# Kernel optimization log

Hardware: AMD Instinct MI355X
Metric: run time of the kernel (lower is better)

Reference implementation:

```python
import jax, jax.numpy as jnp
import numpy as np

NEG_SLOPE = 0.2  # PyG GATConv default LeakyReLU slope


def gat_conv(x, edge_index, W, att_src, att_dst, bias):
    """Faithful PyG GATConv (concat=True, add_self_loops=True).
    x: [N, F_in]; W: [F_in, H*C]; att_src/att_dst: [H, C]; bias: [H*C].
    Returns [N, H*C].
    """
    N = x.shape[0]
    H, C = att_src.shape
    loops = jnp.arange(N, dtype=edge_index.dtype)
    src = jnp.concatenate([edge_index[0], loops])  # message sources
    dst = jnp.concatenate([edge_index[1], loops])  # message targets

    h = (x @ W).reshape(N, H, C)                         # [N,H,C]
    a_src = jnp.sum(h * att_src[None], axis=-1)          # [N,H]
    a_dst = jnp.sum(h * att_dst[None], axis=-1)          # [N,H]

    e = jax.nn.leaky_relu(a_src[src] + a_dst[dst], NEG_SLOPE)   # [E,H]
    # segment softmax over incoming edges of each dst node
    m = jax.ops.segment_max(e, dst, num_segments=N)             # [N,H]
    e = jnp.exp(e - m[dst])
    denom = jax.ops.segment_sum(e, dst, num_segments=N)         # [N,H]
    alpha = e / denom[dst]                                      # [E,H]

    msg = h[src] * alpha[:, :, None]                            # [E,H,C]
    out = jax.ops.segment_sum(msg, dst, num_segments=N)         # [N,H,C]
    return out.reshape(N, H * C) + bias


def setup_inputs() -> dict:
    key = jax.random.key(0)
    ks = jax.random.split(key, 12)
    N, F_in, HID, H, CLS = 50000, 128, 64, 4, 40
    E = 800000
    x = jax.random.normal(ks[0], (N, F_in), dtype=jnp.float32)
    edge_index = jax.random.randint(ks[1], (2, E), 0, N, dtype=jnp.int64)
    s = 0.1
    return {
        "x": x,
        "edge_index": edge_index,
        "W1": jax.random.normal(ks[2], (F_in, H * HID), jnp.float32) * s,
        "att_src1": jax.random.normal(ks[3], (H, HID), jnp.float32) * s,
        "att_dst1": jax.random.normal(ks[4], (H, HID), jnp.float32) * s,
        "b1": jnp.zeros((H * HID,), jnp.float32),
        "W2": jax.random.normal(ks[5], (H * HID, H * CLS), jnp.float32) * s,
        "att_src2": jax.random.normal(ks[6], (H, CLS), jnp.float32) * s,
        "att_dst2": jax.random.normal(ks[7], (H, CLS), jnp.float32) * s,
        "b2": jnp.zeros((H * CLS,), jnp.float32),
    }


def reference(x, edge_index, W1, att_src1, att_dst1, b1, W2, att_src2, att_dst2, b2):
    # feature standardization (torch.std is unbiased, ddof=1)
    mean = jnp.mean(x, axis=0)
    std = jnp.std(x, axis=0, ddof=1)
    x = (x - mean) / std
    x = gat_conv(x, edge_index, W1, att_src1, att_dst1, b1)
    x = jax.nn.relu(x)
    # dropout p=0.4 is identity in eval mode
    x = gat_conv(x, edge_index, W2, att_src2, att_dst2, b2)
    return x
```

## Files before the change

### kernel.cpp

```cpp
#include <hip/hip_runtime.h>
#include <math.h>

#define NEG_SLOPE 0.2f

constexpr int F_IN  = 128;
constexpr int HC1   = 256;
constexpr int HC2   = 160;
constexpr int NHEAD = 4;
constexpr int EB    = 2048;
constexpr int NPB   = 256;
constexpr int BCAP  = 8192;

typedef _Float16 h8v __attribute__((ext_vector_type(8)));
typedef _Float16 h4v __attribute__((ext_vector_type(4)));
typedef _Float16 h2v __attribute__((ext_vector_type(2)));
typedef float f4v __attribute__((ext_vector_type(4)));

#define FMIX_LO(acc, pk, wt) \
    asm("v_fma_mix_f32 %0, %1, %2, %0 op_sel:[0,0,0] op_sel_hi:[1,0,0]" \
        : "+v"(acc) : "v"(pk), "v"(wt))
#define FMIX_HI(acc, pk, wt) \
    asm("v_fma_mix_f32 %0, %1, %2, %0 op_sel:[1,0,0] op_sel_hi:[1,0,0]" \
        : "+v"(acc) : "v"(pk), "v"(wt))

__device__ __forceinline__ int edge_val(const void* p, int m64, long long i) {
    if (m64) return (int)((const long long*)p)[i];
    return ((const int*)p)[i];
}

__global__ void detect_kernel(const unsigned int* __restrict__ ei_words, int* __restrict__ mode,
                              float* __restrict__ stats) {
    stats[threadIdx.x] = 0.f;
    __shared__ unsigned int red[256];
    unsigned int v = 0;
    for (int i = 1 + 2 * (int)threadIdx.x; i < 4096; i += 512) v |= ei_words[i];
    red[threadIdx.x] = v;
    __syncthreads();
    for (int off = 128; off > 0; off >>= 1) {
        if (threadIdx.x < off) red[threadIdx.x] |= red[threadIdx.x + off];
        __syncthreads();
    }
    if (threadIdx.x == 0) *mode = (red[0] == 0u) ? 1 : 0;
}

__global__ __launch_bounds__(256) void fused_pre_kernel(
    const void* __restrict__ ei, const int* __restrict__ mode, int E, int nbuck, int nblk1,
    int* __restrict__ hist, const float* __restrict__ x, float* __restrict__ stats, int N,
    const float* __restrict__ W1, const float* __restrict__ aS1, const float* __restrict__ aD1,
    _Float16* __restrict__ B1x, const float* __restrict__ W2, const float* __restrict__ aS2,
    const float* __restrict__ aD2, _Float16* __restrict__ B2x, int nbStats) {
    int b = blockIdx.x;
    if (b < nblk1) {
        __shared__ int lh[256];
        for (int i = threadIdx.x; i < nbuck; i += 256) lh[i] = 0;
        __syncthreads();
        int m = *mode;
        long long e0 = (long long)b * EB;
#pragma unroll
        for (int k = 0; k < EB / 256; k++) {
            long long e = e0 + (int)threadIdx.x + k * 256;
            if (e < E) {
                int d = edge_val(ei, m, (long long)E + e);
                atomicAdd(&lh[d >> 8], 1);
            }
        }
        __syncthreads();
        for (int i = threadIdx.x; i < nbuck; i += 256) hist[(size_t)i * nblk1 + b] = lh[i];
    } else if (b < nblk1 + nbStats) {
        int t = (int)threadIdx.x;
        int c = t & 31;
        int g = t >> 5;
        int r0 = (b - nblk1) * 256;
        int rend = min(r0 + 256, N);
        f4v s = {0.f, 0.f, 0.f, 0.f}, q = {0.f, 0.f, 0.f, 0.f};
        for (int r = r0 + g; r < rend; r += 8) {
            f4v v = *(const f4v*)&x[(long)r * F_IN + 4 * c];
            s += v;
            q += v * v;
        }
        __shared__ f4v sh4[256];
        sh4[t] = s;
        __syncthreads();
        if (t < 32) {
            f4v a = sh4[t];
            for (int g2 = 1; g2 < 8; g2++) a += sh4[g2 * 32 + t];
            atomicAdd(&stats[4 * t + 0], a[0]);
            atomicAdd(&stats[4 * t + 1], a[1]);
            atomicAdd(&stats[4 * t + 2], a[2]);
            atomicAdd(&stats[4 * t + 3], a[3]);
        }
        __syncthreads();
        sh4[t] = q;
        __syncthreads();
        if (t < 32) {
            f4v a = sh4[t];
            for (int g2 = 1; g2 < 8; g2++) a += sh4[g2 * 32 + t];
            atomicAdd(&stats[128 + 4 * t + 0], a[0]);
            atomicAdd(&stats[128 + 4 * t + 1], a[1]);
            atomicAdd(&stats[128 + 4 * t + 2], a[2]);
            atomicAdd(&stats[128 + 4 * t + 3], a[3]);
        }
    } else {
        constexpr int T1 = (HC1 + 16) * F_IN;
        constexpr int T2 = (HC2 + 16) * HC1;
        int idx = (b - nblk1 - nbStats) * 256 + (int)threadIdx.x;
        if (idx < T1) {
            int n = idx / F_IN, k = idx - n * F_IN;
            float v = 0.f;
            if (n < HC1) {
                v = W1[k * HC1 + n];
            } else {
                int n2 = n - HC1;
                if (n2 < 8) {
                    int hd = n2 & 3;
                    const float* a = (n2 < 4) ? aS1 : aD1;
                    for (int c = 0; c < 64; c++) v += W1[k * HC1 + hd * 64 + c] * a[hd * 64 + c];
                }
            }
            B1x[n * F_IN + k] = (_Float16)v;
        } else if (idx < T1 + T2) {
            int i2 = idx - T1;
            int n = i2 / HC1, k = i2 - n * HC1;
            float v = 0.f;
            if (n < HC2) {
                v = W2[k * HC2 + n];
            } else {
                int n2 = n - HC2;
                if (n2 < 8) {
                    int hd = n2 & 3;
                    const float* a = (n2 < 4) ? aS2 : aD2;
                    for (int c = 0; c < 40; c++) v += W2[k * HC2 + hd * 40 + c] * a[hd * 40 + c];
                }
            }
            B2x[n * HC1 + k] = (_Float16)v;
        }
    }
}

__global__ __launch_bounds__(256) void fused_mid_kernel(
    const float* __restrict__ x, const float* __restrict__ stats, _Float16* __restrict__ xs,
    int total4, float invN, float invN1, const int* __restrict__ hist,
    int* __restrict__ colBaseT, int* __restrict__ bucketTotal, int nbuck, int nblk1,
    int nbStd) {
    int b = blockIdx.x;
    if (b < nbStd) {
        int i = b * 256 + (int)threadIdx.x;
        if (i >= total4) return;
        int c = (i * 4) & (F_IN - 1);
        float4 s4 = *(const float4*)&stats[c];
        float4 q4 = *(const float4*)&stats[128 + c];
        float4 v = ((const float4*)x)[i];
        h4v o;
        o[0] = (_Float16)((v.x - s4.x * invN) / sqrtf((q4.x - s4.x * s4.x * invN) * invN1));
        o[1] = (_Float16)((v.y - s4.y * invN) / sqrtf((q4.y - s4.y * s4.y * invN) * invN1));
        o[2] = (_Float16)((v.z - s4.z * invN) / sqrtf((q4.z - s4.z * s4.z * invN) * invN1));
        o[3] = (_Float16)((v.w - s4.w * invN) / sqrtf((q4.w - s4.w * s4.w * invN) * invN1));
        ((h4v*)xs)[i] = o;
    } else {
        int bb = b - nbStd;
        int t = (int)threadIdx.x;
        __shared__ int sh[512];
        __shared__ int wsum[4];
        for (int i = t; i < nblk1; i += 256) sh[i] = hist[(size_t)bb * nblk1 + i];
        __syncthreads();
        int carry = 0;
        for (int base = 0; base < nblk1; base += 256) {
            int idx = base + t;
            int v = (idx < nblk1) ? sh[idx] : 0;
            int lane = t & 63, w = t >> 6;
            int xv = v;
#pragma unroll
            for (int d = 1; d < 64; d <<= 1) {
                int y = __shfl_up(xv, d);
                if (lane >= d) xv += y;
            }
            if (lane == 63) wsum[w] = xv;
            __syncthreads();
            int wb = 0;
            for (int k = 0; k < w; k++) wb += wsum[k];
            int excl = xv - v + wb + carry;
            if (idx < nblk1) colBaseT[(size_t)idx * nbuck + bb] = excl;
            carry += wsum[0] + wsum[1] + wsum[2] + wsum[3];
            __syncthreads();
        }
        if (t == 0) bucketTotal[bb] = carry;
    }
}

__global__ __launch_bounds__(256) void scatter1_kernel(const void* __restrict__ ei,
                                                       const int* __restrict__ mode, int E,
                                                       int nbuck,
                                                       const int* __restrict__ colBaseT,
                                                       int* __restrict__ bucketEdges) {
    __shared__ int cur[256];
    int b = blockIdx.x;
    for (int i = threadIdx.x; i < nbuck; i += 256)
        cur[i] = colBaseT[(size_t)b * nbuck + i];
    __syncthreads();
    int m = *mode;
    long long e0 = (long long)b * EB;
#pragma unroll
    for (int k = 0; k < EB / 256; k++) {
        long long e = e0 + (int)threadIdx.x + k * 256;
        if (e < E) {
            int s = edge_val(ei, m, e);
            int d = edge_val(ei, m, (long long)E + e);
            int bk = d >> 8;
            int r = atomicAdd(&cur[bk], 1);
            bucketEdges[(size_t)bk * BCAP + r] = s | ((d & (NPB - 1)) << 16);
        }
    }
}

__global__ __launch_bounds__(256) void bucket_count_scan_kernel(
    const int* __restrict__ bucketEdges, const int* __restrict__ bucketTotal,
    int* __restrict__ offsets, int* __restrict__ blocksum, int N) {
    __shared__ int c[NPB];
    int b = blockIdx.x, t = threadIdx.x;
    c[t] = 0;
    __syncthreads();
    int cnt = bucketTotal[b];
    const int* be = bucketEdges + (size_t)b * BCAP;
    for (int i = t; i < cnt; i += 256) atomicAdd(&c[(be[i] >> 16) & (NPB - 1)], 1);
    __syncthreads();
    int node = b * NPB + t;
    int v = (node < N) ? c[t] + 1 : 0;
    int lane = t & 63, w = t >> 6;
    int xv = v;
#pragma unroll
    for (int d = 1; d < 64; d <<= 1) {
        int y = __shfl_up(xv, d);
        if (lane >= d) xv += y;
    }
    __shared__ int wsum[4];
    if (lane == 63) wsum[w] = xv;
    __syncthreads();
    int base = 0;
    for (int k = 0; k < w; k++) base += wsum[k];
    int incl = xv + base;
    if (node < N) offsets[node + 1] = incl;
    if (t == 255) blocksum[b] = incl;
}

__global__ void scan_add_kernel(const int* __restrict__ blocksum, int* __restrict__ offsets, int N,
                                int nb) {
    int t = threadIdx.x;
    int v = (t < nb) ? blocksum[t] : 0;
    int lane = t & 63, w = t >> 6;
    int x = v;
#pragma unroll
    for (int d = 1; d < 64; d <<= 1) {
        int y = __shfl_up(x, d);
        if (lane >= d) x += y;
    }
    __shared__ int wsum[4];
    __shared__ int excl[256];
    if (lane == 63) wsum[w] = x;
    __syncthreads();
    int base = 0;
    for (int k = 0; k < w; k++) base += wsum[k];
    excl[t] = x + base - v;
    __syncthreads();
    int myb = excl[blockIdx.x];
    int i = blockIdx.x * 256 + t;
    if (i < N) offsets[i + 1] += myb;
    if (i == 0) offsets[0] = 0;
}

__device__ __forceinline__ void att1_body(int blk, const _Float16* __restrict__ A,
                                          const _Float16* __restrict__ Batt,
                                          float* __restrict__ as_, float* __restrict__ ad_,
                                          int M) {
    constexpr int KT = F_IN / 32;
    int w = threadIdx.x >> 6;
    int l = threadIdx.x & 63;
    int quad = l >> 4, lan = l & 15;
    int row = blk * 64 + w * 16 + lan;
    int arow = min(row, M - 1);
    const _Float16* Aptr = A + (long)arow * F_IN + quad * 8;
    h8v afr[KT], bfr[KT];
#pragma unroll
    for (int k0 = 0; k0 < KT; k0++) afr[k0] = *(const h8v*)(Aptr + k0 * 32);
#pragma unroll
    for (int k0 = 0; k0 < KT; k0++)
        bfr[k0] = *(const h8v*)(Batt + (long)lan * F_IN + k0 * 32 + quad * 8);
    f4v acc = {0.f, 0.f, 0.f, 0.f};
#pragma unroll
    for (int k0 = 0; k0 < KT; k0++)
        acc = __builtin_amdgcn_mfma_f32_16x16x32_f16(afr[k0], bfr[k0], acc, 0, 0, 0);
    int orow = blk * 64 + w * 16 + quad * 4;
#pragma unroll
    for (int r = 0; r < 4; r++) {
        int gr = orow + r;
        if (gr < M) {
            float av = acc[r];
            if (lan < 4)
                as_[gr * 4 + lan] = av;
            else if (lan < 8)
                ad_[gr * 4 + lan - 4] = av;
        }
    }
}

__global__ __launch_bounds__(256) void fused_csr_att1_kernel(
    const int* __restrict__ bucketEdges, const int* __restrict__ bucketTotal,
    const int* __restrict__ offsets, int* __restrict__ csr, int N, int nbuck,
    const _Float16* __restrict__ xs, const _Float16* __restrict__ B1x,
    float* __restrict__ as_, float* __restrict__ ad_) {
    int b = blockIdx.x;
    if (b < nbuck) {
        __shared__ int cur[NPB];
        int t = threadIdx.x;
        int node = b * NPB + t;
        if (node < N) {
            int off = offsets[node];
            csr[off] = node;
            cur[t] = off + 1;
        }
        __syncthreads();
        int cnt = bucketTotal[b];
        const int* be = bucketEdges + (size_t)b * BCAP;
        for (int i = t; i < cnt; i += 256) {
            int v = be[i];
            int pos = atomicAdd(&cur[(v >> 16) & (NPB - 1)], 1);
            csr[pos] = v & 0xFFFF;
        }
    } else {
        att1_body(b - nbuck, xs, B1x + (size_t)HC1 * F_IN, as_, ad_, N);
    }
}

__global__ __launch_bounds__(256, 4) void aggregate_x4_kernel(
    const _Float16* __restrict__ xs, const float* __restrict__ a_src,
    const float* __restrict__ a_dst, const int* __restrict__ offsets,
    const int* __restrict__ csr_src, _Float16* __restrict__ aggx_lo,
    _Float16* __restrict__ aggx_hi, int Ntot) {
    int w = threadIdx.x >> 6, l = threadIdx.x & 63;
    int node = blockIdx.x * 4 + w;
    if (node >= Ntot) return;

    __shared__ __align__(16) int sidx_sh[4][64];
    __shared__ __align__(16) float ew_sh[4][64][4];

    int start = offsets[node], deg = offsets[node + 1] - start;
    float4 adv = ((const float4*)a_dst)[node];
    const char* hbl = (const char*)xs + 4 * l;

    float ds0 = 0.f, ds1 = 0.f, ds2 = 0.f, ds3 = 0.f;
    float a00 = 0.f, a01 = 0.f, a10 = 0.f, a11 = 0.f;
    float a20 = 0.f, a21 = 0.f, a30 = 0.f, a31 = 0.f;

#define X4_EDGE(p, wv)                                   \
    do {                                                 \
        FMIX_LO(a00, p, wv.x); FMIX_HI(a01, p, wv.x);    \
        FMIX_LO(a10, p, wv.y); FMIX_HI(a11, p, wv.y);    \
        FMIX_LO(a20, p, wv.z); FMIX_HI(a21, p, wv.z);    \
        FMIX_LO(a30, p, wv.w); FMIX_HI(a31, p, wv.w);    \
    } while (0)

    for (int base = 0; base < deg; base += 64) {
        int cnt = min(64, deg - base);
        if (l < cnt) {
            int s = csr_src[start + base + l];
            sidx_sh[w][l] = s * (F_IN * 2);
            float4 av = ((const float4*)a_src)[s];
            float e0 = av.x + adv.x, e1 = av.y + adv.y, e2 = av.z + adv.z, e3 = av.w + adv.w;
            e0 = fmaxf(e0, NEG_SLOPE * e0);
            e1 = fmaxf(e1, NEG_SLOPE * e1);
            e2 = fmaxf(e2, NEG_SLOPE * e2);
            e3 = fmaxf(e3, NEG_SLOPE * e3);
            float w0 = __expf(e0), w1 = __expf(e1), w2 = __expf(e2), w3 = __expf(e3);
            *(float4*)ew_sh[w][l] = make_float4(w0, w1, w2, w3);
            ds0 += w0;
            ds1 += w1;
            ds2 += w2;
            ds3 += w3;
        }
        int j = 0;
        for (; j + 3 < cnt; j += 4) {
            int4 o4 = *(const int4*)&sidx_sh[w][j];
            float4 wa = *(const float4*)ew_sh[w][j + 0];
            float4 wb = *(const float4*)ew_sh[w][j + 1];
            float4 wc = *(const float4*)ew_sh[w][j + 2];
            float4 wd = *(const float4*)ew_sh[w][j + 3];
            int p0 = *(const int*)(hbl + o4.x);
            int p1 = *(const int*)(hbl + o4.y);
            int p2 = *(const int*)(hbl + o4.z);
            int p3 = *(const int*)(hbl + o4.w);
            X4_EDGE(p0, wa);
            X4_EDGE(p1, wb);
            X4_EDGE(p2, wc);
            X4_EDGE(p3, wd);
        }
        for (; j < cnt; j++) {
            int off = sidx_sh[w][j];
            float4 wa = *(const float4*)ew_sh[w][j];
            int p0 = *(const int*)(hbl + off);
            X4_EDGE(p0, wa);
        }
    }
#undef X4_EDGE

#pragma unroll
    for (int off = 1; off < 64; off <<= 1) {
        ds0 += __shfl_xor(ds0, off);
        ds1 += __shfl_xor(ds1, off);
        ds2 += __shfl_xor(ds2, off);
        ds3 += __shfl_xor(ds3, off);
    }

    float i0 = 1.0f / ds0, i1 = 1.0f / ds1, i2 = 1.0f / ds2, i3 = 1.0f / ds3;
    h2v hv;
    hv[0] = (_Float16)(a00 * i0);
    hv[1] = (_Float16)(a01 * i0);
    *(h2v*)(aggx_lo + (size_t)node * F_IN + 2 * l) = hv;
    hv[0] = (_Float16)(a10 * i1);
    hv[1] = (_Float16)(a11 * i1);
    *(h2v*)(aggx_lo + ((size_t)Ntot + node) * F_IN + 2 * l) = hv;
    hv[0] = (_Float16)(a20 * i2);
    hv[1] = (_Float16)(a21 * i2);
    *(h2v*)(aggx_hi + (size_t)node * F_IN + 2 * l) = hv;
    hv[0] = (_Float16)(a30 * i3);
    hv[1] = (_Float16)(a31 * i3);
    *(h2v*)(aggx_hi + ((size_t)Ntot + node) * F_IN + 2 * l) = hv;
}

template <int CT0, int CT1>
__device__ __forceinline__ void gemm1b_lds_body(int blk, const _Float16* __restrict__ Ah,
                                                const _Float16* __restrict__ Btx,
                                                _Float16* Bs, const float* __restrict__ bias,
                                                _Float16* __restrict__ C_, int M) {
    constexpr int NC = CT1 - CT0;
    constexpr int KT = F_IN / 32;
    int t = threadIdx.x;
    int w = t >> 6, l = t & 63;
    int quad = l >> 4, lan = l & 15;
    int row = blk * 64 + w * 16 + lan;
    int arow = min(row, M - 1);
    const _Float16* A0 = Ah + (size_t)arow * F_IN + quad * 8;
    const _Float16* A1 = Ah + ((size_t)M + arow) * F_IN + quad * 8;
    h8v af0[KT], af1[KT];
#pragma unroll
    for (int k0 = 0; k0 < KT; k0++) af0[k0] = *(const h8v*)(A0 + k0 * 32);
#pragma unroll
    for (int k0 = 0; k0 < KT; k0++) af1[k0] = *(const h8v*)(A1 + k0 * 32);
#pragma unroll
    for (int jj = 0; jj < NC * KT * 64 / 256; jj++) {
        int j = jj * 256 + t;
        int cik = j >> 6;
        int k0_ = cik % KT, ci_ = cik / KT;
        int jl = j & 63;
        const _Float16* src =
            Btx + (long)((CT0 + ci_) * 16 + (jl & 15)) * F_IN + k0_ * 32 + (jl >> 4) * 8;
        *(h8v*)(Bs + (size_t)j * 8) = *(const h8v*)src;
    }
    __syncthreads();
    f4v acc[NC] = {};
#pragma unroll
    for (int k0 = 0; k0 < KT; k0++)
#pragma unroll
        for (int ci = 0; ci < NC; ci++) {
            h8v bf = *(const h8v*)(Bs + ((size_t)(ci * KT + k0) * 64 + l) * 8);
            h8v af = (ci < 4) ? af0[k0] : af1[k0];
            acc[ci] = __builtin_amdgcn_mfma_f32_16x16x32_f16(af, bf, acc[ci], 0, 0, 0);
        }
    int orow = blk * 64 + w * 16 + quad * 4;
#pragma unroll
    for (int r = 0; r < 4; r++) {
        int gr = orow + r;
        if (gr < M) {
            _Float16* out = C_ + (long)gr * HC1 + lan;
#pragma unroll
            for (int ci = 0; ci < NC; ci++) {
                int ct = CT0 + ci;
                float v = acc[ci][r] + bias[ct * 16 + lan];
                out[ct * 16] = (_Float16)fmaxf(v, 0.f);
            }
        }
    }
}

__global__ __launch_bounds__(256, 3) void gemm1b_kernel(const _Float16* __restrict__ Alo,
                                                        const _Float16* __restrict__ Ahi,
                                                        const _Float16* __restrict__ Btx,
                                                        const float* __restrict__ bias,
                                                        _Float16* __restrict__ C_, int M) {
    __shared__ __align__(16) _Float16 Bs[8 * 4 * 64 * 8];
    int blk = blockIdx.x >> 1;
    if (blockIdx.x & 1)
        gemm1b_lds_body<8, 16>(blk, Ahi, Btx, Bs, bias, C_, M);
    else
        gemm1b_lds_body<0, 8>(blk, Alo, Btx, Bs, bias, C_, M);
}

template <int CT0, int CT1>
__device__ __forceinline__ void gemm2_lds_body(int blk, const _Float16* __restrict__ A,
                                               const _Float16* __restrict__ Btx,
                                               _Float16* Bs, _Float16* __restrict__ C_,
                                               float* __restrict__ as_, float* __restrict__ ad_,
                                               int M) {
    constexpr int NT = HC2 / 16;
    constexpr int NC = CT1 - CT0;
    constexpr int KT = HC1 / 32;
    int t = threadIdx.x;
    int w = t >> 6, l = t & 63;
    int quad = l >> 4, lan = l & 15;
    int row = blk * 64 + w * 16 + lan;
    int arow = min(row, M - 1);
    const _Float16* Aptr = A + (long)arow * HC1 + quad * 8;
    h8v afr[KT];
#pragma unroll
    for (int k0 = 0; k0 < KT; k0++) afr[k0] = *(const h8v*)(Aptr + k0 * 32);
#pragma unroll
    for (int jj = 0; jj < NC * KT * 64 / 256; jj++) {
        int j = jj * 256 + t;
        int cik = j >> 6;
        int k0_ = cik % KT, ci_ = cik / KT;
        int jl = j & 63;
        const _Float16* src =
            Btx + (long)((CT0 + ci_) * 16 + (jl & 15)) * HC1 + k0_ * 32 + (jl >> 4) * 8;
        *(h8v*)(Bs + (size_t)j * 8) = *(const h8v*)src;
    }
    __syncthreads();
    f4v acc[NC] = {};
#pragma unroll
    for (int k0 = 0; k0 < KT; k0++)
#pragma unroll
        for (int ci = 0; ci < NC; ci++) {
            h8v bf = *(const h8v*)(Bs + ((size_t)(ci * KT + k0) * 64 + l) * 8);
            acc[ci] = __builtin_amdgcn_mfma_f32_16x16x32_f16(afr[k0], bf, acc[ci], 0, 0, 0);
        }
    int orow = blk * 64 + w * 16 + quad * 4;
#pragma unroll
    for (int r = 0; r < 4; r++) {
        int gr = orow + r;
        if (gr < M) {
            _Float16* out = C_ + (long)gr * HC2 + lan;
#pragma unroll
            for (int ci = 0; ci < NC; ci++) {
                int ct = CT0 + ci;
                if (ct < NT) out[ct * 16] = (_Float16)acc[ci][r];
            }
            if (CT1 == NT + 1) {
                float av = acc[NC - 1][r];
                if (lan < 4)
                    as_[gr * 4 + lan] = av;
                else if (lan < 8)
                    ad_[gr * 4 + lan - 4] = av;
            }
        }
    }
}

__global__ __launch_bounds__(256, 3) void gemm2_kernel(const _Float16* __restrict__ A,
                                                       const _Float16* __restrict__ B2x,
                                                       _Float16* __restrict__ C_,
                                                       float* __restrict__ as_,
                                                       float* __restrict__ ad_, int M) {
    __shared__ __align__(16) _Float16 Bs[6 * 8 * 64 * 8];
    int blk = blockIdx.x >> 1;
    if (blockIdx.x & 1)
        gemm2_lds_body<5, 11>(blk, A, B2x, Bs, C_, as_, ad_, M);
    else
        gemm2_lds_body<0, 5>(blk, A, B2x, Bs, C_, as_, ad_, M);
}

template <int HC, bool RELU, typename OutT>
__global__ __launch_bounds__(256, 4) void aggregate_kernel(
    const _Float16* __restrict__ hb, const float* __restrict__ a_src,
    const float* __restrict__ a_dst, const int* __restrict__ offsets,
    const int* __restrict__ csr_src, const float* __restrict__ bias, OutT* __restrict__ out,
    int Ntot) {
    constexpr int ACT = HC / 4;
    constexpr int CHPH = HC / NHEAD;
    constexpr bool FULL = (ACT == 64);
    int w = threadIdx.x >> 6, l = threadIdx.x & 63;
    int node = blockIdx.x * 4 + w;
    if (node >= Ntot) return;

    __shared__ __align__(16) int sidx_sh[4][64];
    __shared__ __align__(16) float ew_sh[4][64][4];

    int start = offsets[node], end = offsets[node + 1];
    int deg = end - start;
    float4 adv = ((const float4*)a_dst)[node];
    const int hd = min((4 * l) / CHPH, 3);
    const char* hbl = (const char*)hb + 8 * l;

    float ds0 = 0.f, ds1 = 0.f, ds2 = 0.f, ds3 = 0.f;
    float a0 = 0.f, a1 = 0.f, a2 = 0.f, a3 = 0.f;

    for (int base = 0; base < deg; base += 64) {
        int cnt = min(64, deg - base);
        if (l < cnt) {
            int s = csr_src[start + base + l];
            sidx_sh[w][l] = s * (HC * 2);
            float4 av = ((const float4*)a_src)[s];
            float e0 = av.x + adv.x, e1 = av.y + adv.y, e2 = av.z + adv.z, e3 = av.w + adv.w;
            e0 = fmaxf(e0, NEG_SLOPE * e0);
            e1 = fmaxf(e1, NEG_SLOPE * e1);
            e2 = fmaxf(e2, NEG_SLOPE * e2);
            e3 = fmaxf(e3, NEG_SLOPE * e3);
            float w0 = __expf(e0), w1 = __expf(e1), w2 = __expf(e2), w3 = __expf(e3);
            *(float4*)ew_sh[w][l] = make_float4(w0, w1, w2, w3);
            ds0 += w0;
            ds1 += w1;
            ds2 += w2;
            ds3 += w3;
        }
        int j = 0;
        for (; j + 7 < cnt; j += 8) {
            int4 oa = *(const int4*)&sidx_sh[w][j];
            int4 ob = *(const int4*)&sidx_sh[w][j + 4];
            float w0 = ew_sh[w][j + 0][hd], w1 = ew_sh[w][j + 1][hd];
            float w2 = ew_sh[w][j + 2][hd], w3 = ew_sh[w][j + 3][hd];
            float w4 = ew_sh[w][j + 4][hd], w5 = ew_sh[w][j + 5][hd];
            float w6 = ew_sh[w][j + 6][hd], w7 = ew_sh[w][j + 7][hd];
            if (FULL || l < ACT) {
                int2 p0 = *(const int2*)(hbl + oa.x);
                int2 p1 = *(const int2*)(hbl + oa.y);
                int2 p2 = *(const int2*)(hbl + oa.z);
                int2 p3 = *(const int2*)(hbl + oa.w);
                int2 p4 = *(const int2*)(hbl + ob.x);
                int2 p5 = *(const int2*)(hbl + ob.y);
                int2 p6 = *(const int2*)(hbl + ob.z);
                int2 p7 = *(const int2*)(hbl + ob.w);
                FMIX_LO(a0, p0.x, w0); FMIX_HI(a1, p0.x, w0);
                FMIX_LO(a2, p0.y, w0); FMIX_HI(a3, p0.y, w0);
                FMIX_LO(a0, p1.x, w1); FMIX_HI(a1, p1.x, w1);
                FMIX_LO(a2, p1.y, w1); FMIX_HI(a3, p1.y, w1);
                FMIX_LO(a0, p2.x, w2); FMIX_HI(a1, p2.x, w2);
                FMIX_LO(a2, p2.y, w2); FMIX_HI(a3, p2.y, w2);
                FMIX_LO(a0, p3.x, w3); FMIX_HI(a1, p3.x, w3);
                FMIX_LO(a2, p3.y, w3); FMIX_HI(a3, p3.y, w3);
                FMIX_LO(a0, p4.x, w4); FMIX_HI(a1, p4.x, w4);
                FMIX_LO(a2, p4.y, w4); FMIX_HI(a3, p4.y, w4);
                FMIX_LO(a0, p5.x, w5); FMIX_HI(a1, p5.x, w5);
                FMIX_LO(a2, p5.y, w5); FMIX_HI(a3, p5.y, w5);
                FMIX_LO(a0, p6.x, w6); FMIX_HI(a1, p6.x, w6);
                FMIX_LO(a2, p6.y, w6); FMIX_HI(a3, p6.y, w6);
                FMIX_LO(a0, p7.x, w7); FMIX_HI(a1, p7.x, w7);
                FMIX_LO(a2, p7.y, w7); FMIX_HI(a3, p7.y, w7);
            }
        }
        for (; j + 3 < cnt; j += 4) {
            int4 o4 = *(const int4*)&sidx_sh[w][j];
            float w0 = ew_sh[w][j + 0][hd], w1 = ew_sh[w][j + 1][hd];
            float w2 = ew_sh[w][j + 2][hd], w3 = ew_sh[w][j + 3][hd];
            if (FULL || l < ACT) {
                int2 p0 = *(const int2*)(hbl + o4.x);
                int2 p1 = *(const int2*)(hbl + o4.y);
                int2 p2 = *(const int2*)(hbl + o4.z);
                int2 p3 = *(const int2*)(hbl + o4.w);
                FMIX_LO(a0, p0.x, w0); FMIX_HI(a1, p0.x, w0);
                FMIX_LO(a2, p0.y, w0); FMIX_HI(a3, p0.y, w0);
                FMIX_LO(a0, p1.x, w1); FMIX_HI(a1, p1.x, w1);
                FMIX_LO(a2, p1.y, w1); FMIX_HI(a3, p1.y, w1);
                FMIX_LO(a0, p2.x, w2); FMIX_HI(a1, p2.x, w2);
                FMIX_LO(a2, p2.y, w2); FMIX_HI(a3, p2.y, w2);
                FMIX_LO(a0, p3.x, w3); FMIX_HI(a1, p3.x, w3);
                FMIX_LO(a2, p3.y, w3); FMIX_HI(a3, p3.y, w3);
            }
        }
        for (; j < cnt; j++) {
            int off = sidx_sh[w][j];
            float w0 = ew_sh[w][j][hd];
            if (FULL || l < ACT) {
                int2 p0 = *(const int2*)(hbl + off);
                FMIX_LO(a0, p0.x, w0); FMIX_HI(a1, p0.x, w0);
                FMIX_LO(a2, p0.y, w0); FMIX_HI(a3, p0.y, w0);
            }
        }
    }

#pragma unroll
    for (int off = 1; off < 64; off <<= 1) {
        ds0 += __shfl_xor(ds0, off);
        ds1 += __shfl_xor(ds1, off);
        ds2 += __shfl_xor(ds2, off);
        ds3 += __shfl_xor(ds3, off);
    }

    if (FULL || l < ACT) {
        float dsel = hd == 0 ? ds0 : hd == 1 ? ds1 : hd == 2 ? ds2 : ds3;
        float inv = 1.0f / dsel;
        float4 bv = ((const float4*)bias)[l];
        float r0 = a0 * inv + bv.x;
        float r1 = a1 * inv + bv.y;
        float r2 = a2 * inv + bv.z;
        float r3 = a3 * inv + bv.w;
        if (RELU) {
            r0 = fmaxf(r0, 0.f);
            r1 = fmaxf(r1, 0.f);
            r2 = fmaxf(r2, 0.f);
            r3 = fmaxf(r3, 0.f);
        }
        OutT* op = out + (long)node * HC + 4 * l;
        if (sizeof(OutT) == 2) {
            h4v hv;
            hv[0] = (_Float16)r0;
            hv[1] = (_Float16)r1;
            hv[2] = (_Float16)r2;
            hv[3] = (_Float16)r3;
            *(h4v*)op = hv;
        } else {
            *(float4*)op = make_float4(r0, r1, r2, r3);
        }
    }
}

extern "C" void kernel_launch(void* const* d_in, const int* in_sizes, int n_in, void* d_out,
                              int out_size, void* d_ws, size_t ws_size, hipStream_t stream) {
    const float* x = (const float*)d_in[0];
    const void* ei = d_in[1];
    const float* W1 = (const float*)d_in[2];
    const float* attS1 = (const float*)d_in[3];
    const float* attD1 = (const float*)d_in[4];
    const float* b1 = (const float*)d_in[5];
    const float* W2 = (const float*)d_in[6];
    const float* attS2 = (const float*)d_in[7];
    const float* attD2 = (const float*)d_in[8];
    const float* b2 = (const float*)d_in[9];
    float* out = (float*)d_out;

    int N = in_sizes[0] / F_IN;
    int E = in_sizes[1] / 2;
    int nb = (N + 255) / 256;
    int nw = (N + 3) / 4;
    int nblk1 = (E + EB - 1) / EB;
    int nbuck = (N + NPB - 1) / NPB;

    _Float16* xs_h = (_Float16*)d_ws;
    _Float16* o1h = xs_h + (size_t)N * F_IN;
    _Float16* hb2 = o1h + (size_t)N * HC1;
    _Float16* aggx_hi = hb2 + (size_t)N * HC2;
    _Float16* B1x = aggx_hi + (size_t)N * HC1;
    _Float16* B2x = B1x + (HC1 + 16) * F_IN;
    float* as1 = (float*)(B2x + (HC2 + 16) * HC1);
    float* ad1 = as1 + (size_t)N * NHEAD;
    float* as2 = ad1 + (size_t)N * NHEAD;
    float* ad2 = as2 + (size_t)N * NHEAD;
    float* stats = ad2 + (size_t)N * NHEAD;
    int* offsets = (int*)(stats + 256);
    int* csr = offsets + (N + 4);
    int* blocksum = csr + (E + N);
    int* mode = blocksum + 256;
    int* bucketEdges = (int*)o1h;
    int* hist = bucketEdges + (size_t)nbuck * BCAP;
    int* colBaseT = hist + (size_t)nbuck * nblk1;
    int* bucketTotal = colBaseT + (size_t)nblk1 * nbuck;
    _Float16* aggx_lo = (_Float16*)d_out;

    constexpr int TCV = (HC1 + 16) * F_IN + (HC2 + 16) * HC1;
    int nbConv = (TCV + 255) / 256;
    int total4 = N * F_IN / 4;
    int nbStd = (total4 + 255) / 256;
    int nbG1 = (N + 63) / 64;

    detect_kernel<<<1, 256, 0, stream>>>((const unsigned int*)ei, mode, stats);
    fused_pre_kernel<<<nblk1 + nb + nbConv, 256, 0, stream>>>(
        ei, mode, E, nbuck, nblk1, hist, x, stats, N, W1, attS1, attD1, B1x, W2, attS2, attD2,
        B2x, nb);
    fused_mid_kernel<<<nbStd + nbuck, 256, 0, stream>>>(x, stats, xs_h, total4,
                                                        1.0f / (float)N, 1.0f / (float)(N - 1),
                                                        hist, colBaseT, bucketTotal, nbuck,
                                                        nblk1, nbStd);
    scatter1_kernel<<<nblk1, 256, 0, stream>>>(ei, mode, E, nbuck, colBaseT, bucketEdges);
    bucket_count_scan_kernel<<<nbuck, 256, 0, stream>>>(bucketEdges, bucketTotal, offsets,
                                                        blocksum, N);
    scan_add_kernel<<<nb, 256, 0, stream>>>(blocksum, offsets, N, nb);
    fused_csr_att1_kernel<<<nbuck + nbG1, 256, 0, stream>>>(bucketEdges, bucketTotal, offsets,
                                                            csr, N, nbuck, xs_h, B1x, as1, ad1);
    aggregate_x4_kernel<<<nw, 256, 0, stream>>>(xs_h, as1, ad1, offsets, csr, aggx_lo, aggx_hi,
                                                N);
    gemm1b_kernel<<<nbG1 * 2, 256, 0, stream>>>(aggx_lo, aggx_hi, B1x, b1, o1h, N);
    gemm2_kernel<<<nbG1 * 2, 256, 0, stream>>>(o1h, B2x, hb2, as2, ad2, N);
    aggregate_kernel<HC2, false, float>
        <<<nw, 256, 0, stream>>>(hb2, as2, ad2, offsets, csr, b2, out, N);
}
```

Before: 292.2 us.

## Fuse layer-1 aggregation with per-node projection GEMM via shared memory

```diff
diff --git a/kernel.cpp b/kernel.cpp
--- a/kernel.cpp
+++ b/kernel.cpp
@@ -330,21 +330,18 @@
     }
 }
 
-__global__ __launch_bounds__(256, 4) void aggregate_x4_kernel(
+__global__ __launch_bounds__(256, 4) void aggregate_x4g_kernel(
     const _Float16* __restrict__ xs, const float* __restrict__ a_src,
     const float* __restrict__ a_dst, const int* __restrict__ offsets,
-    const int* __restrict__ csr_src, _Float16* __restrict__ aggx_lo,
-    _Float16* __restrict__ aggx_hi, int Ntot) {
+    const int* __restrict__ csr_src, const _Float16* __restrict__ B1x,
+    const float* __restrict__ bias, _Float16* __restrict__ o1, int Ntot) {
     int w = threadIdx.x >> 6, l = threadIdx.x & 63;
     int node = blockIdx.x * 4 + w;
-    if (node >= Ntot) return;
+    const bool valid = (node < Ntot);
 
     __shared__ __align__(16) int sidx_sh[4][64];
     __shared__ __align__(16) float ew_sh[4][64][4];
-
-    int start = offsets[node], deg = offsets[node + 1] - start;
-    float4 adv = ((const float4*)a_dst)[node];
-    const char* hbl = (const char*)xs + 4 * l;
+    __shared__ __align__(16) _Float16 agg_sh[4][NHEAD][F_IN];
 
     float ds0 = 0.f, ds1 = 0.f, ds2 = 0.f, ds3 = 0.f;
     float a00 = 0.f, a01 = 0.f, a10 = 0.f, a11 = 0.f;
@@ -358,139 +355,102 @@
         FMIX_LO(a30, p, wv.w); FMIX_HI(a31, p, wv.w);    \
     } while (0)
 
-    for (int base = 0; base < deg; base += 64) {
-        int cnt = min(64, deg - base);
-        if (l < cnt) {
-            int s = csr_src[start + base + l];
-            sidx_sh[w][l] = s * (F_IN * 2);
-            float4 av = ((const float4*)a_src)[s];
-            float e0 = av.x + adv.x, e1 = av.y + adv.y, e2 = av.z + adv.z, e3 = av.w + adv.w;
-            e0 = fmaxf(e0, NEG_SLOPE * e0);
-            e1 = fmaxf(e1, NEG_SLOPE * e1);
-            e2 = fmaxf(e2, NEG_SLOPE * e2);
-            e3 = fmaxf(e3, NEG_SLOPE * e3);
-            float w0 = __expf(e0), w1 = __expf(e1), w2 = __expf(e2), w3 = __expf(e3);
-            *(float4*)ew_sh[w][l] = make_float4(w0, w1, w2, w3);
-            ds0 += w0;
-            ds1 += w1;
-            ds2 += w2;
-            ds3 += w3;
-        }
-        int j = 0;
-        for (; j + 3 < cnt; j += 4) {
-            int4 o4 = *(const int4*)&sidx_sh[w][j];
-            float4 wa = *(const float4*)ew_sh[w][j + 0];
-            float4 wb = *(const float4*)ew_sh[w][j + 1];
-            float4 wc = *(const float4*)ew_sh[w][j + 2];
-            float4 wd = *(const float4*)ew_sh[w][j + 3];
-            int p0 = *(const int*)(hbl + o4.x);
-            int p1 = *(const int*)(hbl + o4.y);
-            int p2 = *(const int*)(hbl + o4.z);
-            int p3 = *(const int*)(hbl + o4.w);
-            X4_EDGE(p0, wa);
-            X4_EDGE(p1, wb);
-            X4_EDGE(p2, wc);
-            X4_EDGE(p3, wd);
-        }
-        for (; j < cnt; j++) {
-            int off = sidx_sh[w][j];
-            float4 wa = *(const float4*)ew_sh[w][j];
-            int p0 = *(const int*)(hbl + off);
-            X4_EDGE(p0, wa);
-        }
+    if (valid) {
+        int start = offsets[node], deg = offsets[node + 1] - start;
+        float4 adv = ((const float4*)a_dst)[node];
+        const char* hbl = (const char*)xs + 4 * l;
+
+        for (int base = 0; base < deg; base += 64) {
+            int cnt = min(64, deg - base);
+            if (l < cnt) {
+                int s = csr_src[start + base + l];
+                sidx_sh[w][l] = s * (F_IN * 2);
+                float4 av = ((const float4*)a_src)[s];
+                float e0 = av.x + adv.x, e1 = av.y + adv.y, e2 = av.z + adv.z,
+                      e3 = av.w + adv.w;
+                e0 = fmaxf(e0, NEG_SLOPE * e0);
+                e1 = fmaxf(e1, NEG_SLOPE * e1);
+                e2 = fmaxf(e2, NEG_SLOPE * e2);
+                e3 = fmaxf(e3, NEG_SLOPE * e3);
+                float w0 = __expf(e0), w1 = __expf(e1), w2 = __expf(e2), w3 = __expf(e3);
+                *(float4*)ew_sh[w][l] = make_float4(w0, w1, w2, w3);
+                ds0 += w0;
+                ds1 += w1;
+                ds2 += w2;
+                ds3 += w3;
+            }
+            int j = 0;
+            for (; j + 3 < cnt; j += 4) {
+                int4 o4 = *(const int4*)&sidx_sh[w][j];
+                float4 wa = *(const float4*)ew_sh[w][j + 0];
+                float4 wb = *(const float4*)ew_sh[w][j + 1];
+                float4 wc = *(const float4*)ew_sh[w][j + 2];
+                float4 wd = *(const float4*)ew_sh[w][j + 3];
+                int p0 = *(const int*)(hbl + o4.x);
+                int p1 = *(const int*)(hbl + o4.y);
+                int p2 = *(const int*)(hbl + o4.z);
+                int p3 = *(const int*)(hbl + o4.w);
+                X4_EDGE(p0, wa);
+                X4_EDGE(p1, wb);
+                X4_EDGE(p2, wc);
+                X4_EDGE(p3, wd);
+            }
+            for (; j < cnt; j++) {
+                int off = sidx_sh[w][j];
+                float4 wa = *(const float4*)ew_sh[w][j];
+                int p0 = *(const int*)(hbl + off);
+                X4_EDGE(p0, wa);
+            }
+        }
+
+#pragma unroll
+        for (int off = 1; off < 64; off <<= 1) {
+            ds0 += __shfl_xor(ds0, off);
+            ds1 += __shfl_xor(ds1, off);
+            ds2 += __shfl_xor(ds2, off);
+            ds3 += __shfl_xor(ds3, off);
+        }
+
+        float i0 = 1.0f / ds0, i1 = 1.0f / ds1, i2 = 1.0f / ds2, i3 = 1.0f / ds3;
+        h2v hv;
+        hv[0] = (_Float16)(a00 * i0);
+        hv[1] = (_Float16)(a01 * i0);
+        *(h2v*)&agg_sh[w][0][2 * l] = hv;
+        hv[0] = (_Float16)(a10 * i1);
+        hv[1] = (_Float16)(a11 * i1);
+        *(h2v*)&agg_sh[w][1][2 * l] = hv;
+        hv[0] = (_Float16)(a20 * i2);
+        hv[1] = (_Float16)(a21 * i2);
+        *(h2v*)&agg_sh[w][2][2 * l] = hv;
+        hv[0] = (_Float16)(a30 * i3);
+        hv[1] = (_Float16)(a31 * i3);
+        *(h2v*)&agg_sh[w][3][2 * l] = hv;
     }
 #undef X4_EDGE
 
-#pragma unroll
-    for (int off = 1; off < 64; off <<= 1) {
-        ds0 += __shfl_xor(ds0, off);
-        ds1 += __shfl_xor(ds1, off);
-        ds2 += __shfl_xor(ds2, off);
-        ds3 += __shfl_xor(ds3, off);
-    }
-
-    float i0 = 1.0f / ds0, i1 = 1.0f / ds1, i2 = 1.0f / ds2, i3 = 1.0f / ds3;
-    h2v hv;
-    hv[0] = (_Float16)(a00 * i0);
-    hv[1] = (_Float16)(a01 * i0);
-    *(h2v*)(aggx_lo + (size_t)node * F_IN + 2 * l) = hv;
-    hv[0] = (_Float16)(a10 * i1);
-    hv[1] = (_Float16)(a11 * i1);
-    *(h2v*)(aggx_lo + ((size_t)Ntot + node) * F_IN + 2 * l) = hv;
-    hv[0] = (_Float16)(a20 * i2);
-    hv[1] = (_Float16)(a21 * i2);
-    *(h2v*)(aggx_hi + (size_t)node * F_IN + 2 * l) = hv;
-    hv[0] = (_Float16)(a30 * i3);
-    hv[1] = (_Float16)(a31 * i3);
-    *(h2v*)(aggx_hi + ((size_t)Ntot + node) * F_IN + 2 * l) = hv;
-}
-
-template <int CT0, int CT1>
-__device__ __forceinline__ void gemm1b_lds_body(int blk, const _Float16* __restrict__ Ah,
-                                                const _Float16* __restrict__ Btx,
-                                                _Float16* Bs, const float* __restrict__ bias,
-                                                _Float16* __restrict__ C_, int M) {
-    constexpr int NC = CT1 - CT0;
-    constexpr int KT = F_IN / 32;
-    int t = threadIdx.x;
-    int w = t >> 6, l = t & 63;
-    int quad = l >> 4, lan = l & 15;
-    int row = blk * 64 + w * 16 + lan;
-    int arow = min(row, M - 1);
-    const _Float16* A0 = Ah + (size_t)arow * F_IN + quad * 8;
-    const _Float16* A1 = Ah + ((size_t)M + arow) * F_IN + quad * 8;
-    h8v af0[KT], af1[KT];
-#pragma unroll
-    for (int k0 = 0; k0 < KT; k0++) af0[k0] = *(const h8v*)(A0 + k0 * 32);
-#pragma unroll
-    for (int k0 = 0; k0 < KT; k0++) af1[k0] = *(const h8v*)(A1 + k0 * 32);
-#pragma unroll
-    for (int jj = 0; jj < NC * KT * 64 / 256; jj++) {
-        int j = jj * 256 + t;
-        int cik = j >> 6;
-        int k0_ = cik % KT, ci_ = cik / KT;
-        int jl = j & 63;
-        const _Float16* src =
-            Btx + (long)((CT0 + ci_) * 16 + (jl & 15)) * F_IN + k0_ * 32 + (jl >> 4) * 8;
-        *(h8v*)(Bs + (size_t)j * 8) = *(const h8v*)src;
-    }
-    __syncthreads();
-    f4v acc[NC] = {};
-#pragma unroll
-    for (int k0 = 0; k0 < KT; k0++)
-#pragma unroll
-        for (int ci = 0; ci < NC; ci++) {
-            h8v bf = *(const h8v*)(Bs + ((size_t)(ci * KT + k0) * 64 + l) * 8);
-            h8v af = (ci < 4) ? af0[k0] : af1[k0];
-            acc[ci] = __builtin_amdgcn_mfma_f32_16x16x32_f16(af, bf, acc[ci], 0, 0, 0);
-        }
-    int orow = blk * 64 + w * 16 + quad * 4;
-#pragma unroll
-    for (int r = 0; r < 4; r++) {
-        int gr = orow + r;
-        if (gr < M) {
-            _Float16* out = C_ + (long)gr * HC1 + lan;
-#pragma unroll
-            for (int ci = 0; ci < NC; ci++) {
-                int ct = CT0 + ci;
-                float v = acc[ci][r] + bias[ct * 16 + lan];
-                out[ct * 16] = (_Float16)fmaxf(v, 0.f);
-            }
-        }
-    }
-}
-
-__global__ __launch_bounds__(256, 3) void gemm1b_kernel(const _Float16* __restrict__ Alo,
-                                                        const _Float16* __restrict__ Ahi,
-                                                        const _Float16* __restrict__ Btx,
-                                                        const float* __restrict__ bias,
-                                                        _Float16* __restrict__ C_, int M) {
-    __shared__ __align__(16) _Float16 Bs[8 * 4 * 64 * 8];
-    int blk = blockIdx.x >> 1;
-    if (blockIdx.x & 1)
-        gemm1b_lds_body<8, 16>(blk, Ahi, Btx, Bs, bias, C_, M);
-    else
-        gemm1b_lds_body<0, 8>(blk, Alo, Btx, Bs, bias, C_, M);
+    __syncthreads();
+
+    int c = threadIdx.x;
+    int hd2 = c >> 6;
+    const _Float16* wcol = B1x + (size_t)c * F_IN;
+    h8v wv[16];
+#pragma unroll
+    for (int kk = 0; kk < 16; kk++) wv[kk] = *(const h8v*)(wcol + kk * 8);
+    float bc = bias[c];
+#pragma unroll
+    for (int n = 0; n < 4; n++) {
+        int gn = blockIdx.x * 4 + n;
+        if (gn < Ntot) {
+            float acc = 0.f;
+#pragma unroll
+            for (int kk = 0; kk < 16; kk++) {
+                h8v av = *(const h8v*)&agg_sh[n][hd2][kk * 8];
+#pragma unroll
+                for (int e = 0; e < 8; e++) acc += (float)av[e] * (float)wv[kk][e];
+            }
+            o1[(size_t)gn * HC1 + c] = (_Float16)fmaxf(acc + bc, 0.f);
+        }
+    }
 }
 
 template <int CT0, int CT1>
@@ -733,8 +693,7 @@
     _Float16* xs_h = (_Float16*)d_ws;
     _Float16* o1h = xs_h + (size_t)N * F_IN;
     _Float16* hb2 = o1h + (size_t)N * HC1;
-    _Float16* aggx_hi = hb2 + (size_t)N * HC2;
-    _Float16* B1x = aggx_hi + (size_t)N * HC1;
+    _Float16* B1x = hb2 + (size_t)N * HC2;
     _Float16* B2x = B1x + (HC1 + 16) * F_IN;
     float* as1 = (float*)(B2x + (HC2 + 16) * HC1);
     float* ad1 = as1 + (size_t)N * NHEAD;
@@ -749,7 +708,6 @@
     int* hist = bucketEdges + (size_t)nbuck * BCAP;
     int* colBaseT = hist + (size_t)nbuck * nblk1;
     int* bucketTotal = colBaseT + (size_t)nblk1 * nbuck;
-    _Float16* aggx_lo = (_Float16*)d_out;
 
     constexpr int TCV = (HC1 + 16) * F_IN + (HC2 + 16) * HC1;
     int nbConv = (TCV + 255) / 256;
@@ -771,9 +729,8 @@
     scan_add_kernel<<<nb, 256, 0, stream>>>(blocksum, offsets, N, nb);
     fused_csr_att1_kernel<<<nbuck + nbG1, 256, 0, stream>>>(bucketEdges, bucketTotal, offsets,
                                                             csr, N, nbuck, xs_h, B1x, as1, ad1);
-    aggregate_x4_kernel<<<nw, 256, 0, stream>>>(xs_h, as1, ad1, offsets, csr, aggx_lo, aggx_hi,
-                                                N);
-    gemm1b_kernel<<<nbG1 * 2, 256, 0, stream>>>(aggx_lo, aggx_hi, B1x, b1, o1h, N);
+    aggregate_x4g_kernel<<<nw, 256, 0, stream>>>(xs_h, as1, ad1, offsets, csr, B1x, b1, o1h,
+                                                 N);
     gemm2_kernel<<<nbG1 * 2, 256, 0, stream>>>(o1h, B2x, hb2, as2, ad2, N);
     aggregate_kernel<HC2, false, float>
         <<<nw, 256, 0, stream>>>(hb2, as2, ad2, offsets, csr, b2, out, N);
```

Result: slower. 379.5 us (+29.9%).
